# Performance work log

Hardware: AMD Instinct MI355X
Metric: run time of the kernel (lower is better)

Reference implementation:

```python
import jax, jax.numpy as jnp
import numpy as np

N_USERS = 100_000
N_ITEMS = 100_000
D = 64            # args.in_size == args.out_size (GraphConv has weight=None)
N_INTENTS = 128   # hardcoded in DCCF
HID = 128         # SemanticAttention hidden_size
N_UI_EDGES = 1_000_000
N_MP_EDGES = 500_000
N_MP = 2          # metapaths per node type
B = 4096
N_LAYERS = 2      # hardcoded in DCCF


def setup_inputs() -> dict:
    key = jax.random.key(0)
    ks = jax.random.split(key, 20)
    s = 0.1
    inp = {}
    inp['user_feat'] = jax.random.normal(ks[0], (N_USERS, D), jnp.float32) * s
    inp['item_feat'] = jax.random.normal(ks[1], (N_ITEMS, D), jnp.float32) * s
    inp['user_intent'] = jax.random.normal(ks[2], (D, N_INTENTS), jnp.float32) * s
    inp['item_intent'] = jax.random.normal(ks[3], (D, N_INTENTS), jnp.float32) * s
    inp['sa_u_W1'] = jax.random.normal(ks[4], (D, HID), jnp.float32) * s
    inp['sa_u_b1'] = jnp.zeros((HID,), jnp.float32)
    inp['sa_u_w2'] = jax.random.normal(ks[5], (HID,), jnp.float32) * s
    inp['sa_i_W1'] = jax.random.normal(ks[6], (D, HID), jnp.float32) * s
    inp['sa_i_b1'] = jnp.zeros((HID,), jnp.float32)
    inp['sa_i_w2'] = jax.random.normal(ks[7], (HID,), jnp.float32) * s
    inp['ui_src'] = jax.random.randint(ks[8], (N_UI_EDGES,), 0, N_USERS)
    inp['ui_dst'] = jax.random.randint(ks[9], (N_UI_EDGES,), 0, N_ITEMS)
    inp['mp_user'] = jax.random.randint(ks[10], (N_MP, 2, N_MP_EDGES), 0, N_USERS)
    inp['mp_item'] = jax.random.randint(ks[11], (N_MP, 2, N_MP_EDGES), 0, N_ITEMS)
    # indices drawn WITHOUT replacement so torch.unique(index) in ssl_loss is a no-op
    inp['user_idx'] = jax.random.choice(ks[12], N_USERS, (B,), replace=False)
    inp['item_idx'] = jax.random.choice(ks[13], N_ITEMS, (B,), replace=False)
    inp['neg_item_idx'] = jax.random.randint(ks[14], (B,), 0, N_ITEMS)
    return inp


def _forward(user_feat, item_feat, user_intent, item_intent,
             sa_u_W1, sa_u_b1, sa_u_w2, sa_i_W1, sa_i_b1, sa_i_w2,
             ui_src, ui_dst, mp_user, mp_item, user_idx, item_idx, neg_item_idx):
    n_nodes = N_USERS + N_ITEMS
    # symmetric bipartite adjacency in COO (tmp_adj + tmp_adj.T)
    rows = jnp.concatenate([ui_src, ui_dst + N_USERS])
    cols = jnp.concatenate([ui_dst + N_USERS, ui_src])
    deg = jnp.maximum(jax.ops.segment_sum(jnp.ones_like(rows, jnp.float32), rows,
                                          num_segments=n_nodes), 1.0)
    dinv = jax.lax.rsqrt(deg)
    gv = dinv[rows] * dinv[cols]  # G = D^{-1/2} A D^{-1/2}

    def spmm(x):  # gather-scale-scatter, the torch_sparse.spmm
        return jax.ops.segment_sum(gv[:, None] * x[cols], rows, num_segments=n_nodes)

    # ---- DCCF ----
    emb = jnp.concatenate([user_feat, item_feat], axis=0)
    total = emb
    for _ in range(N_LAYERS):
        gnn = spmm(emb)
        u, it = emb[:N_USERS], emb[N_USERS:]
        u_int = jax.nn.softmax(u @ user_intent, axis=1) @ user_intent.T
        i_int = jax.nn.softmax(it @ item_intent, axis=1) @ item_intent.T
        emb = gnn + jnp.concatenate([u_int, i_int], axis=0) + emb
        total = total + emb  # torch.stack(...).sum(dim=1)
    ua, ia = total[:N_USERS], total[N_USERS:]

    # ---- HANLayer: GraphConv(norm='both', weight=None) per metapath ----
    def graphconv(src, dst, h, n):
        ones = jnp.ones_like(src, jnp.float32)
        outdeg = jnp.maximum(jax.ops.segment_sum(ones, src, num_segments=n), 1.0)
        indeg = jnp.maximum(jax.ops.segment_sum(ones, dst, num_segments=n), 1.0)
        x = h * jax.lax.rsqrt(outdeg)[:, None]
        agg = jax.ops.segment_sum(x[src], dst, num_segments=n)
        return agg * jax.lax.rsqrt(indeg)[:, None]

    def sem_att(z, W1, b1, w2):  # z: [N, M, D]
        w = jnp.mean(jnp.tanh(z @ W1 + b1) @ w2, axis=0)  # [M]
        beta = jax.nn.softmax(w)
        return jnp.einsum('m,nmd->nd', beta, z)

    zu = jnp.stack([graphconv(mp_user[m, 0], mp_user[m, 1], user_feat, N_USERS)
                    for m in range(N_MP)], axis=1)
    h2_u = sem_att(zu, sa_u_W1, sa_u_b1, sa_u_w2)
    zi = jnp.stack([graphconv(mp_item[m, 0], mp_item[m, 1], item_feat, N_ITEMS)
                    for m in range(N_MP)], axis=1)
    h2_i = sem_att(zi, sa_i_W1, sa_i_b1, sa_i_w2)

    user_emb = 0.5 * ua + 0.5 * h2_u
    item_emb = 0.5 * ia + 0.5 * h2_i

    def ssl(d1, d2, idx):  # InfoNCE with temp 0.5 (idx already unique)
        e1 = d1[idx]
        e2 = d2[idx]
        e1 = e1 / jnp.linalg.norm(e1, axis=1, keepdims=True)
        e2 = e2 / jnp.linalg.norm(e2, axis=1, keepdims=True)
        pos = jnp.sum(e1 * e2, axis=1) / 0.5
        lse = jax.nn.logsumexp(e1 @ e2.T / 0.5, axis=1)
        return -jnp.sum(pos - lse) / idx.shape[0]

    ssl_loss = ssl(h2_u, ua, user_idx) + ssl(h2_i, ia, item_idx)
    return (user_emb[user_idx], item_emb[item_idx], item_emb[neg_item_idx], ssl_loss)


def reference(user_feat, item_feat, user_intent, item_intent,
              sa_u_W1, sa_u_b1, sa_u_w2, sa_i_W1, sa_i_b1, sa_i_w2,
              ui_src, ui_dst, mp_user, mp_item, user_idx, item_idx, neg_item_idx):
    return _forward(user_feat, item_feat, user_intent, item_intent,
                    sa_u_W1, sa_u_b1, sa_u_w2, sa_i_W1, sa_i_b1, sa_i_w2,
                    ui_src, ui_dst, mp_user, mp_item, user_idx, item_idx, neg_item_idx)
```

## Files before the change

kernel.cpp:

```cpp
#include <hip/hip_runtime.h>
#include <math.h>

#define NUSERS   100000
#define NITEMS   100000
#define NNODES   200000
#define DD       64
#define NI       128
#define E_UI     1000000
#define E_MP     500000
#define BB       4096
#define NSTRIP   6250

#define O_CNT       0LL
#define O_OUTCNT    600000LL
#define O_CURSOR    1000000LL
#define O_PARTIALS  1600000LL
#define O_UITB_U    1625600LL
#define O_UITB_I    1629696LL
#define O_UIB_U     1633792LL
#define O_UIB_I     1637888LL
#define O_W1B_U     1641984LL
#define O_W1B_I     1646080LL
#define O_SUMEXP    1700000LL
#define O_POS       1708192LL
#define ZEND        1716384LL
#define O_OFF       1716384LL
#define O_BSUM      2316448LL
#define O_DINV      2317472LL
#define O_OINV      2517472LL
#define O_IINV      2917472LL
#define O_ADJ       3317472LL
#define O_WSUM      7317472LL
#define O_EMBA      7317480LL
#define O_TOTAL     20117480LL
#define O_EMBB      32917480LL
#define O_E1U       45717480LL
#define O_E2U       45979624LL
#define O_E1I       46241768LL
#define O_E2I       46503912LL

typedef __attribute__((ext_vector_type(8))) short short8;
typedef __attribute__((ext_vector_type(4))) float f32x4;

__device__ __forceinline__ short f2bf(float x) {
  unsigned u = __float_as_uint(x);
  unsigned r = (u + 0x7FFFu + ((u >> 16) & 1u)) >> 16;
  return (short)r;
}

__global__ void k_hist_main(const int* __restrict__ src, const int* __restrict__ dst,
                            int* __restrict__ cnt) {
  int e = blockIdx.x * 256 + threadIdx.x;
  if (e < E_UI) {
    atomicAdd(&cnt[src[e]], 1);
    atomicAdd(&cnt[NUSERS + dst[e]], 1);
  }
}

__global__ void k_hist_mp(const int* __restrict__ mpu, const int* __restrict__ mpi,
                          int* __restrict__ cnt, int* __restrict__ outcnt) {
  int e = blockIdx.x * 256 + threadIdx.x;
  int g = blockIdx.y;
  if (e < E_MP) {
    const int* base = (g < 2) ? (mpu + (long long)g * 2 * E_MP)
                              : (mpi + (long long)(g - 2) * 2 * E_MP);
    int s = base[e];
    int d = base[E_MP + e];
    atomicAdd(&outcnt[g * NUSERS + s], 1);
    atomicAdd(&cnt[NNODES + g * NUSERS + d], 1);
  }
}

__global__ __launch_bounds__(1024) void k_scan1(const int* __restrict__ in, int* __restrict__ out,
                                                int* __restrict__ bsum, int n) {
  __shared__ int s[1024];
  int i = blockIdx.x * 1024 + threadIdx.x;
  int v = (i < n) ? in[i] : 0;
  s[threadIdx.x] = v;
  __syncthreads();
  for (int off = 1; off < 1024; off <<= 1) {
    int x = (threadIdx.x >= off) ? s[threadIdx.x - off] : 0;
    __syncthreads();
    s[threadIdx.x] += x;
    __syncthreads();
  }
  if (i < n) out[i] = s[threadIdx.x] - v;
  if (threadIdx.x == 1023) bsum[blockIdx.x] = s[1023];
}

__global__ __launch_bounds__(1024) void k_scan2(int* __restrict__ bsum, int nb) {
  __shared__ int s[1024];
  int v = (threadIdx.x < nb) ? bsum[threadIdx.x] : 0;
  s[threadIdx.x] = v;
  __syncthreads();
  for (int off = 1; off < 1024; off <<= 1) {
    int x = (threadIdx.x >= off) ? s[threadIdx.x - off] : 0;
    __syncthreads();
    s[threadIdx.x] += x;
    __syncthreads();
  }
  if (threadIdx.x < nb) bsum[threadIdx.x] = s[threadIdx.x] - v;
}

__global__ __launch_bounds__(1024) void k_scan3(int* __restrict__ out, const int* __restrict__ bsum, int n) {
  int i = blockIdx.x * 1024 + threadIdx.x;
  if (i < n) out[i] += bsum[blockIdx.x];
}

__global__ void k_inv(const int* __restrict__ cnt, const int* __restrict__ outcnt,
                      float* __restrict__ dinv, float* __restrict__ iinv, float* __restrict__ oinv) {
  int i = blockIdx.x * 256 + threadIdx.x;
  if (i < NNODES) {
    int c = cnt[i]; if (c < 1) c = 1;
    dinv[i] = 1.0f / sqrtf((float)c);
  } else if (i < 600000) {
    int c = cnt[i]; if (c < 1) c = 1;
    iinv[i - NNODES] = 1.0f / sqrtf((float)c);
  }
  if (i < 400000) {
    int c = outcnt[i]; if (c < 1) c = 1;
    oinv[i] = 1.0f / sqrtf((float)c);
  }
}

__global__ void k_scatter_main(const int* __restrict__ src, const int* __restrict__ dst,
                               const int* __restrict__ off, int* __restrict__ cursor,
                               int* __restrict__ adj) {
  int e = blockIdx.x * 256 + threadIdx.x;
  if (e < E_UI) {
    int u = src[e];
    int it = NUSERS + dst[e];
    int p = atomicAdd(&cursor[u], 1);
    adj[off[u] + p] = it;
    int q = atomicAdd(&cursor[it], 1);
    adj[off[it] + q] = u;
  }
}

__global__ void k_scatter_mp(const int* __restrict__ mpu, const int* __restrict__ mpi,
                             const int* __restrict__ off, int* __restrict__ cursor,
                             int* __restrict__ adj) {
  int e = blockIdx.x * 256 + threadIdx.x;
  int g = blockIdx.y;
  if (e < E_MP) {
    const int* base = (g < 2) ? (mpu + (long long)g * 2 * E_MP)
                              : (mpi + (long long)(g - 2) * 2 * E_MP);
    int s = base[e];
    int d = base[E_MP + e];
    int node = NNODES + g * NUSERS + d;
    int p = atomicAdd(&cursor[node], 1);
    adj[off[node] + p] = s;
  }
}

__global__ void k_init(const float4* __restrict__ uf, const float4* __restrict__ itf,
                       float4* __restrict__ emb) {
  int i = blockIdx.x * 256 + threadIdx.x;
  if (i < 3200000) {
    emb[i] = (i < 1600000) ? uf[i] : itf[i - 1600000];
  }
}

__global__ void k_tw(const float* __restrict__ UIu, const float* __restrict__ UIi,
                     const float* __restrict__ W1u, const float* __restrict__ W1i,
                     short* __restrict__ UITBu, short* __restrict__ UITBi,
                     short* __restrict__ UIBu,  short* __restrict__ UIBi,
                     short* __restrict__ W1Bu,  short* __restrict__ W1Bi) {
  int t = blockIdx.x * 256 + threadIdx.x;
  if (t < 8192) {
    int d = t >> 7, j = t & 127;
    UITBu[j * 64 + d] = f2bf(UIu[t]);
    UITBi[j * 64 + d] = f2bf(UIi[t]);
    UIBu[t] = f2bf(UIu[t]);
    UIBi[t] = f2bf(UIi[t]);
    W1Bu[j * 64 + d] = f2bf(W1u[t]);
    W1Bi[j * 64 + d] = f2bf(W1i[t]);
  }
}

__device__ __forceinline__ float acc8(const float* __restrict__ tbl, int miv, float mwv,
                                      int rem, int lane, float acc) {
  unsigned wb = __float_as_uint(mwv);
  for (int k = 0; k < rem; k += 8) {
    int n0 = __builtin_amdgcn_readlane(miv, k + 0);
    int n1 = __builtin_amdgcn_readlane(miv, k + 1);
    int n2 = __builtin_amdgcn_readlane(miv, k + 2);
    int n3 = __builtin_amdgcn_readlane(miv, k + 3);
    int n4 = __builtin_amdgcn_readlane(miv, k + 4);
    int n5 = __builtin_amdgcn_readlane(miv, k + 5);
    int n6 = __builtin_amdgcn_readlane(miv, k + 6);
    int n7 = __builtin_amdgcn_readlane(miv, k + 7);
    float w0 = __uint_as_float(__builtin_amdgcn_readlane(wb, k + 0));
    float w1 = __uint_as_float(__builtin_amdgcn_readlane(wb, k + 1));
    float w2 = __uint_as_float(__builtin_amdgcn_readlane(wb, k + 2));
    float w3 = __uint_as_float(__builtin_amdgcn_readlane(wb, k + 3));
    float w4 = __uint_as_float(__builtin_amdgcn_readlane(wb, k + 4));
    float w5 = __uint_as_float(__builtin_amdgcn_readlane(wb, k + 5));
    float w6 = __uint_as_float(__builtin_amdgcn_readlane(wb, k + 6));
    float w7 = __uint_as_float(__builtin_amdgcn_readlane(wb, k + 7));
    float v0 = tbl[((long long)n0 << 6) + lane], v1 = tbl[((long long)n1 << 6) + lane];
    float v2 = tbl[((long long)n2 << 6) + lane], v3 = tbl[((long long)n3 << 6) + lane];
    float v4 = tbl[((long long)n4 << 6) + lane], v5 = tbl[((long long)n5 << 6) + lane];
    float v6 = tbl[((long long)n6 << 6) + lane], v7 = tbl[((long long)n7 << 6) + lane];
    acc += w0 * v0; acc += w1 * v1; acc += w2 * v2; acc += w3 * v3;
    acc += w4 * v4; acc += w5 * v5; acc += w6 * v6; acc += w7 * v7;
  }
  return acc;
}

template <int R>
__device__ __forceinline__ float acc8f(const float* __restrict__ tbl, int miv, float mwv,
                                       int lane) {
  unsigned wb = __float_as_uint(mwv);
  float acc = 0.0f;
#pragma unroll
  for (int k = 0; k < R; k += 8) {
    int n0 = __builtin_amdgcn_readlane(miv, k + 0);
    int n1 = __builtin_amdgcn_readlane(miv, k + 1);
    int n2 = __builtin_amdgcn_readlane(miv, k + 2);
    int n3 = __builtin_amdgcn_readlane(miv, k + 3);
    int n4 = __builtin_amdgcn_readlane(miv, k + 4);
    int n5 = __builtin_amdgcn_readlane(miv, k + 5);
    int n6 = __builtin_amdgcn_readlane(miv, k + 6);
    int n7 = __builtin_amdgcn_readlane(miv, k + 7);
    float w0 = __uint_as_float(__builtin_amdgcn_readlane(wb, k + 0));
    float w1 = __uint_as_float(__builtin_amdgcn_readlane(wb, k + 1));
    float w2 = __uint_as_float(__builtin_amdgcn_readlane(wb, k + 2));
    float w3 = __uint_as_float(__builtin_amdgcn_readlane(wb, k + 3));
    float w4 = __uint_as_float(__builtin_amdgcn_readlane(wb, k + 4));
    float w5 = __uint_as_float(__builtin_amdgcn_readlane(wb, k + 5));
    float w6 = __uint_as_float(__builtin_amdgcn_readlane(wb, k + 6));
    float w7 = __uint_as_float(__builtin_amdgcn_readlane(wb, k + 7));
    float v0 = tbl[((long long)n0 << 6) + lane], v1 = tbl[((long long)n1 << 6) + lane];
    float v2 = tbl[((long long)n2 << 6) + lane], v3 = tbl[((long long)n3 << 6) + lane];
    float v4 = tbl[((long long)n4 << 6) + lane], v5 = tbl[((long long)n5 << 6) + lane];
    float v6 = tbl[((long long)n6 << 6) + lane], v7 = tbl[((long long)n7 << 6) + lane];
    acc += w0 * v0; acc += w1 * v1; acc += w2 * v2; acc += w3 * v3;
    acc += w4 * v4; acc += w5 * v5; acc += w6 * v6; acc += w7 * v7;
  }
  return acc;
}

__device__ __forceinline__ float gather_tail(const float* __restrict__ tbl,
                                             const int* __restrict__ adj,
                                             int start, int c,
                                             const float* __restrict__ warr, int wofs,
                                             int lane, float acc) {
  for (int kb = 64; kb < c; kb += 64) {
    int rem = c - kb; if (rem > 64) rem = 64;
    int ti = 0; float tw = 0.0f;
    if (lane < rem) { ti = adj[start + kb + lane]; tw = warr[wofs + ti]; }
    acc = acc8(tbl, ti, tw, rem, lane, acc);
  }
  return acc;
}

__device__ __forceinline__ float gather_node(const float* __restrict__ tbl,
                                             const int* __restrict__ adj,
                                             int ofs, int c, int miv, float mwv,
                                             const float* __restrict__ warr, int wofs,
                                             int lane) {
  if (c <= 8)  return acc8f<8>(tbl, miv, mwv, lane);
  if (c <= 16) return acc8f<16>(tbl, miv, mwv, lane);
  if (c <= 24) return acc8f<24>(tbl, miv, mwv, lane);
  int rem = c < 64 ? c : 64;
  float acc = acc8(tbl, miv, mwv, rem, lane, 0.0f);
  if (c > 64) acc = gather_tail(tbl, adj, ofs, c, warr, wofs, lane, acc);
  return acc;
}

__device__ __forceinline__ void acc4x(const float* __restrict__ tbl, int miv, float mwv,
                                      int rem, int grp, int dq, f32x4& acc) {
  for (int k = 0; k < rem; k += 16) {
    int s0 = k + grp, s1 = k + 4 + grp, s2 = k + 8 + grp, s3 = k + 12 + grp;
    int n0 = __shfl(miv, s0), n1 = __shfl(miv, s1);
    int n2 = __shfl(miv, s2), n3 = __shfl(miv, s3);
    float w0 = __shfl(mwv, s0), w1 = __shfl(mwv, s1);
    float w2 = __shfl(mwv, s2), w3 = __shfl(mwv, s3);
    float4 v0 = *(const float4*)(tbl + ((long long)n0 << 6) + dq);
    float4 v1 = *(const float4*)(tbl + ((long long)n1 << 6) + dq);
    float4 v2 = *(const float4*)(tbl + ((long long)n2 << 6) + dq);
    float4 v3 = *(const float4*)(tbl + ((long long)n3 << 6) + dq);
    acc.x += w0 * v0.x; acc.y += w0 * v0.y; acc.z += w0 * v0.z; acc.w += w0 * v0.w;
    acc.x += w1 * v1.x; acc.y += w1 * v1.y; acc.z += w1 * v1.z; acc.w += w1 * v1.w;
    acc.x += w2 * v2.x; acc.y += w2 * v2.y; acc.z += w2 * v2.z; acc.w += w2 * v2.w;
    acc.x += w3 * v3.x; acc.y += w3 * v3.y; acc.z += w3 * v3.z; acc.w += w3 * v3.w;
  }
}

__device__ __forceinline__ void gather_tail4(const float* __restrict__ tbl,
                                             const int* __restrict__ adj,
                                             int start, int c,
                                             const float* __restrict__ warr, int wofs,
                                             int lane, int grp, int dq, f32x4& acc) {
  for (int kb = 64; kb < c; kb += 64) {
    int rem = c - kb; if (rem > 64) rem = 64;
    int ti = 0; float tw = 0.0f;
    if (lane < rem) { ti = adj[start + kb + lane]; tw = warr[wofs + ti]; }
    acc4x(tbl, ti, tw, rem, grp, dq, acc);
  }
}

__device__ __forceinline__ float bcastf(float x) {
  return __uint_as_float(__builtin_amdgcn_readfirstlane(__float_as_uint(x)));
}

__global__ __launch_bounds__(128, 4) void k_layer(
    const float* __restrict__ ecur, float* __restrict__ enext, float* __restrict__ total,
    const int* __restrict__ adj, const int* __restrict__ off, const int* __restrict__ cnt,
    const float* __restrict__ dinv,
    const short* __restrict__ UITBu, const short* __restrict__ UITBi,
    const short* __restrict__ UIBu,  const short* __restrict__ UIBi, int layer) {
  __shared__ float sZ[2][16 * 68];
  __shared__ short sP[2][16 * 136];
  int w = threadIdx.x >> 6, lane = threadIdx.x & 63;
  int nb = blockIdx.x * 32 + w * 16;
  const short* UITB = (nb < NUSERS) ? UITBu : UITBi;
  const short* UIB  = (nb < NUSERS) ? UIBu  : UIBi;
  float* rowZ = sZ[w];
  short* rowP = sP[w];
  int quad = lane >> 4, mrow = lane & 15;

  const float* vrow = ecur + (((long long)(nb + mrow)) << 6) + quad * 8;
  float4 va0 = *(const float4*)(vrow);
  float4 va1 = *(const float4*)(vrow + 4);
  float4 vc0 = *(const float4*)(vrow + 32);
  float4 vc1 = *(const float4*)(vrow + 36);
  short8 a0 = { f2bf(va0.x), f2bf(va0.y), f2bf(va0.z), f2bf(va0.w),
                f2bf(va1.x), f2bf(va1.y), f2bf(va1.z), f2bf(va1.w) };
  short8 a1 = { f2bf(vc0.x), f2bf(vc0.y), f2bf(vc0.z), f2bf(vc0.w),
                f2bf(vc1.x), f2bf(vc1.y), f2bf(vc1.z), f2bf(vc1.w) };

  {
    int ofs[16], cns[16];
    float dn[16];
    int mi[16]; float mw[16];
#pragma unroll
    for (int m = 0; m < 16; m++) {
      ofs[m] = __builtin_amdgcn_readfirstlane(off[nb + m]);
      cns[m] = __builtin_amdgcn_readfirstlane(cnt[nb + m]);
      dn[m]  = bcastf(dinv[nb + m]);
    }
#pragma unroll
    for (int m = 0; m < 16; m++)
      mi[m] = (lane < cns[m]) ? adj[ofs[m] + lane] : 0;
#pragma unroll
    for (int m = 0; m < 16; m++)
      mw[m] = (lane < cns[m]) ? dinv[mi[m]] : 0.0f;
#pragma unroll
    for (int m = 0; m < 16; m++) {
      float acc = gather_node(ecur, adj, ofs[m], cns[m], mi[m], mw[m], dinv, 0, lane);
      rowZ[m * 68 + lane] = dn[m] * acc;
    }
  }

  float den0 = 0.f, den1 = 0.f, den2 = 0.f, den3 = 0.f;
  short* pw = rowP + (quad * 4) * 136 + mrow;
#pragma unroll
  for (int jt = 0; jt < 8; jt++) {
    const short* wr = UITB + ((jt * 16 + mrow) << 6) + quad * 8;
    short8 b0 = *(const short8*)(wr);
    short8 bh = *(const short8*)(wr + 32);
    f32x4 acc = {0.f, 0.f, 0.f, 0.f};
    acc = __builtin_amdgcn_mfma_f32_16x16x32_bf16(a0, b0, acc, 0, 0, 0);
    acc = __builtin_amdgcn_mfma_f32_16x16x32_bf16(a1, bh, acc, 0, 0, 0);
    float e0 = __expf(acc[0]), e1 = __expf(acc[1]);
    float e2 = __expf(acc[2]), e3 = __expf(acc[3]);
    den0 += e0; den1 += e1; den2 += e2; den3 += e3;
    short* pj = pw + jt * 16;
    pj[0] = f2bf(e0); pj[136] = f2bf(e1); pj[272] = f2bf(e2); pj[408] = f2bf(e3);
  }
  for (int mask = 1; mask <= 8; mask <<= 1) {
    den0 += __shfl_xor(den0, mask); den1 += __shfl_xor(den1, mask);
    den2 += __shfl_xor(den2, mask); den3 += __shfl_xor(den3, mask);
  }
  float rd0 = 1.f / den0, rd1 = 1.f / den1, rd2 = 1.f / den2, rd3 = 1.f / den3;

#pragma unroll
  for (int dt = 0; dt < 4; dt++) {
    f32x4 acc = {0.f, 0.f, 0.f, 0.f};
#pragma unroll
    for (int c = 0; c < 4; c++) {
      const short* pr = rowP + mrow * 136 + c * 32 + quad * 8;
      short8 af = *(const short8*)(pr);
      const short* br = UIB + ((dt * 16 + mrow) << 7) + c * 32 + quad * 8;
      short8 bf = *(const short8*)(br);
      acc = __builtin_amdgcn_mfma_f32_16x16x32_bf16(af, bf, acc, 0, 0, 0);
    }
    int d = dt * 16 + mrow;
#define COMB(r, rd)                                                            \
    { int node = nb + quad * 4 + r;                                            \
      long long base = (((long long)node) << 6) + d;                           \
      float o = acc[r] * rd;                                                   \
      float gn = rowZ[(quad * 4 + r) * 68 + d];                                \
      float vv = ecur[base];                                                   \
      float ne = gn + o + vv;                                                  \
      enext[base] = ne;                                                        \
      total[base] = (layer == 0) ? (vv + ne) : (total[base] + ne); }
    COMB(0, rd0) COMB(1, rd1) COMB(2, rd2) COMB(3, rd3)
#undef COMB
  }
}

__global__ __launch_bounds__(256, 6) void k_mp_gather(
    const float* __restrict__ uf, const float* __restrict__ itf,
    const int* __restrict__ adj, const int* __restrict__ off, const int* __restrict__ cnt,
    const float* __restrict__ oinv, const float* __restrict__ iinv,
    float* __restrict__ zu, float* __restrict__ zi) {
  int g = blockIdx.y;
  const float* feat = (g < 2) ? uf : itf;
  float* zb = (g < 2) ? zu + ((long long)g * NUSERS << 6)
                      : zi + ((long long)(g - 2) * NUSERS << 6);
  int w = threadIdx.x >> 6, lane = threadIdx.x & 63;
  int n0 = (blockIdx.x * 4 + w) * 4;
  int gofs = g * NUSERS;
  int grp = lane >> 4, dq = (lane & 15) << 2;
  int ofs[4], cns[4];
  float iv[4];
  int mi[4]; float mw[4];
#pragma unroll
  for (int m = 0; m < 4; m++) {
    int node = NNODES + gofs + n0 + m;
    ofs[m] = __builtin_amdgcn_readfirstlane(off[node]);
    cns[m] = __builtin_amdgcn_readfirstlane(cnt[node]);
    iv[m]  = bcastf(iinv[gofs + n0 + m]);
  }
#pragma unroll
  for (int m = 0; m < 4; m++)
    mi[m] = (lane < cns[m]) ? adj[ofs[m] + lane] : 0;
#pragma unroll
  for (int m = 0; m < 4; m++)
    mw[m] = (lane < cns[m]) ? oinv[gofs + mi[m]] : 0.0f;
#pragma unroll
  for (int m = 0; m < 4; m++) {
    int c = cns[m];
    f32x4 acc = {0.f, 0.f, 0.f, 0.f};
    if (c <= 16) {
      acc4x(feat, mi[m], mw[m], 16, grp, dq, acc);
    } else {
      int rem = c < 64 ? c : 64;
      acc4x(feat, mi[m], mw[m], rem, grp, dq, acc);
      if (c > 64) gather_tail4(feat, adj, ofs[m], c, oinv, gofs, lane, grp, dq, acc);
    }
    acc.x += __shfl_xor(acc.x, 16); acc.y += __shfl_xor(acc.y, 16);
    acc.z += __shfl_xor(acc.z, 16); acc.w += __shfl_xor(acc.w, 16);
    acc.x += __shfl_xor(acc.x, 32); acc.y += __shfl_xor(acc.y, 32);
    acc.z += __shfl_xor(acc.z, 32); acc.w += __shfl_xor(acc.w, 32);
    if (lane < 16) {
      float s = iv[m];
      float4 o = { acc.x * s, acc.y * s, acc.z * s, acc.w * s };
      *(float4*)&zb[((long long)(n0 + m) << 6) + dq] = o;
    }
  }
}

__global__ __launch_bounds__(256, 4) void k_mp_mlp(
    const float* __restrict__ zu, const float* __restrict__ zi,
    const short* __restrict__ W1Bu, const float* __restrict__ b1u, const float* __restrict__ w2u,
    const short* __restrict__ W1Bi, const float* __restrict__ b1i, const float* __restrict__ w2i,
    float* __restrict__ partials) {
  int g = blockIdx.y;
  const short* W1B = (g < 2) ? W1Bu : W1Bi;
  const float* b1  = (g < 2) ? b1u : b1i;
  const float* w2  = (g < 2) ? w2u : w2i;
  const float* zb  = (g < 2) ? zu + ((long long)g * NUSERS << 6)
                             : zi + ((long long)(g - 2) * NUSERS << 6);
  int w = threadIdx.x >> 6, lane = threadIdx.x & 63;
  int strip = blockIdx.x * 4 + w;
  if (strip >= NSTRIP) return;
  int quad = lane >> 4, mrow = lane & 15;
  const float* zrow = zb + (((long long)(strip * 16 + mrow)) << 6) + quad * 8;
  float4 za0 = *(const float4*)(zrow);
  float4 za1 = *(const float4*)(zrow + 4);
  float4 zc0 = *(const float4*)(zrow + 32);
  float4 zc1 = *(const float4*)(zrow + 36);
  short8 a0 = { f2bf(za0.x), f2bf(za0.y), f2bf(za0.z), f2bf(za0.w),
                f2bf(za1.x), f2bf(za1.y), f2bf(za1.z), f2bf(za1.w) };
  short8 a1 = { f2bf(zc0.x), f2bf(zc0.y), f2bf(zc0.z), f2bf(zc0.w),
                f2bf(zc1.x), f2bf(zc1.y), f2bf(zc1.z), f2bf(zc1.w) };
  float psum = 0.0f;
#pragma unroll
  for (int jt = 0; jt < 8; jt++) {
    const short* wr = W1B + ((jt * 16 + mrow) << 6) + quad * 8;
    short8 b0 = *(const short8*)(wr);
    short8 bh = *(const short8*)(wr + 32);
    f32x4 acc = {0.f, 0.f, 0.f, 0.f};
    acc = __builtin_amdgcn_mfma_f32_16x16x32_bf16(a0, b0, acc, 0, 0, 0);
    acc = __builtin_amdgcn_mfma_f32_16x16x32_bf16(a1, bh, acc, 0, 0, 0);
    int j = jt * 16 + mrow;
    float bj = b1[j], wj = w2[j];
#pragma unroll
    for (int r = 0; r < 4; r++) {
      float s = acc[r] + bj;
      psum += wj * (1.0f - 2.0f / (__expf(2.0f * s) + 1.0f));
    }
  }
  for (int m = 32; m; m >>= 1) psum += __shfl_xor(psum, m);
  if (lane == 0) partials[g * NSTRIP + strip] = psum;
}

__global__ void k_beta(const float* __restrict__ partials, float* __restrict__ wsum) {
  int g = blockIdx.x;
  float s = 0.0f;
  for (int i = threadIdx.x; i < NSTRIP; i += 256) s += partials[g * NSTRIP + i];
  for (int m = 32; m; m >>= 1) s += __shfl_xor(s, m);
  __shared__ float r[4];
  if ((threadIdx.x & 63) == 0) r[threadIdx.x >> 6] = s;
  __syncthreads();
  if (threadIdx.x == 0) wsum[g] = r[0] + r[1] + r[2] + r[3];
}

__global__ __launch_bounds__(256) void k_h2out(
    const float* __restrict__ zu, const float* __restrict__ zi,
    const int* __restrict__ user_idx, const int* __restrict__ item_idx, const int* __restrict__ neg_idx,
    const float* __restrict__ total,
    const float* __restrict__ wsum, float* __restrict__ out,
    short* __restrict__ e1u, short* __restrict__ e2u,
    short* __restrict__ e1i, short* __restrict__ e2i, float* __restrict__ pos) {
  int lane = threadIdx.x & 63;
  int row = (blockIdx.x << 2) + (threadIdx.x >> 6);
  int seg = row >> 12;
  int r = row & 4095;
  int idx;
  const float* zb;
  int gbase;
  if (seg == 0)      { idx = user_idx[r]; zb = zu; gbase = 0; }
  else if (seg == 1) { idx = item_idx[r]; zb = zi; gbase = 2; }
  else               { idx = neg_idx[r];  zb = zi; gbase = 2; }
  int tnode = gbase ? (NUSERS + idx) : idx;
  float t = total[((long long)tnode << 6) + lane];
  float w0 = wsum[gbase] * (1.0f / 100000.0f);
  float w1 = wsum[gbase + 1] * (1.0f / 100000.0f);
  float mb = fmaxf(w0, w1);
  float b0 = expf(w0 - mb), b1 = expf(w1 - mb);
  float bs = b0 + b1;
  b0 /= bs; b1 /= bs;
  float z0 = zb[((long long)idx << 6) + lane];
  float z1 = zb[(((long long)NUSERS + idx) << 6) + lane];
  float h2 = b0 * z0 + b1 * z1;
  out[((long long)row << 6) + lane] = 0.5f * t + 0.5f * h2;
  if (seg < 2) {
    float n1 = h2 * h2, n2 = t * t;
    for (int m = 32; m; m >>= 1) { n1 += __shfl_xor(n1, m); n2 += __shfl_xor(n2, m); }
    n1 = sqrtf(n1); n2 = sqrtf(n2);
    float a = h2 / n1, b = t / n2;
    float d = a * b;
    for (int m = 32; m; m >>= 1) d += __shfl_xor(d, m);
    short* e1 = seg ? e1i : e1u;
    short* e2 = seg ? e2i : e2u;
    e1[((long long)r << 6) + lane] = f2bf(a);
    e2[((long long)r << 6) + lane] = f2bf(b);
    if (lane == 0) pos[seg * BB + r] = 2.0f * d;
  }
}

__global__ __launch_bounds__(256) void k_gemm(const short* __restrict__ e1u, const short* __restrict__ e2u,
                                              const short* __restrict__ e1i, const short* __restrict__ e2i,
                                              float* __restrict__ sumexp) {
  int side = blockIdx.z;
  const short* A = side ? e1i : e1u;
  const short* B = side ? e2i : e2u;
  int w = threadIdx.x >> 6, lane = threadIdx.x & 63;
  int quad = lane >> 4, mrow = lane & 15;
  int rbase = blockIdx.y * 64;
  int cbase = blockIdx.x * 256 + w * 64;

  short8 a0[4], a1[4], b0[4], b1[4];
#pragma unroll
  for (int ri = 0; ri < 4; ri++) {
    const short* ar = A + ((long long)(rbase + ri * 16 + mrow) << 6) + quad * 8;
    a0[ri] = *(const short8*)ar;
    a1[ri] = *(const short8*)(ar + 32);
  }
#pragma unroll
  for (int ci = 0; ci < 4; ci++) {
    const short* br = B + ((long long)(cbase + ci * 16 + mrow) << 6) + quad * 8;
    b0[ci] = *(const short8*)br;
    b1[ci] = *(const short8*)(br + 32);
  }
  float rs0[4] = {0.f, 0.f, 0.f, 0.f};
  float rs1[4] = {0.f, 0.f, 0.f, 0.f};
  float rs2[4] = {0.f, 0.f, 0.f, 0.f};
  float rs3[4] = {0.f, 0.f, 0.f, 0.f};
#pragma unroll
  for (int ri = 0; ri < 4; ri++) {
#pragma unroll
    for (int ci = 0; ci < 4; ci++) {
      f32x4 acc = {0.f, 0.f, 0.f, 0.f};
      acc = __builtin_amdgcn_mfma_f32_16x16x32_bf16(a0[ri], b0[ci], acc, 0, 0, 0);
      acc = __builtin_amdgcn_mfma_f32_16x16x32_bf16(a1[ri], b1[ci], acc, 0, 0, 0);
      float e0 = __expf(2.0f * acc[0]);
      float e1 = __expf(2.0f * acc[1]);
      float e2 = __expf(2.0f * acc[2]);
      float e3 = __expf(2.0f * acc[3]);
      if (ri == 0) { rs0[0] += e0; rs0[1] += e1; rs0[2] += e2; rs0[3] += e3; }
      if (ri == 1) { rs1[0] += e0; rs1[1] += e1; rs1[2] += e2; rs1[3] += e3; }
      if (ri == 2) { rs2[0] += e0; rs2[1] += e1; rs2[2] += e2; rs2[3] += e3; }
      if (ri == 3) { rs3[0] += e0; rs3[1] += e1; rs3[2] += e2; rs3[3] += e3; }
    }
  }
#pragma unroll
  for (int mask = 1; mask <= 8; mask <<= 1) {
#pragma unroll
    for (int r = 0; r < 4; r++) {
      rs0[r] += __shfl_xor(rs0[r], mask);
      rs1[r] += __shfl_xor(rs1[r], mask);
      rs2[r] += __shfl_xor(rs2[r], mask);
      rs3[r] += __shfl_xor(rs3[r], mask);
    }
  }
  if (mrow == 0) {
    float* sb = sumexp + side * BB + rbase + quad * 4;
#pragma unroll
    for (int r = 0; r < 4; r++) {
      __hip_atomic_fetch_add(&sb[r], rs0[r], __ATOMIC_RELAXED, __HIP_MEMORY_SCOPE_AGENT);
      __hip_atomic_fetch_add(&sb[16 + r], rs1[r], __ATOMIC_RELAXED, __HIP_MEMORY_SCOPE_AGENT);
      __hip_atomic_fetch_add(&sb[32 + r], rs2[r], __ATOMIC_RELAXED, __HIP_MEMORY_SCOPE_AGENT);
      __hip_atomic_fetch_add(&sb[48 + r], rs3[r], __ATOMIC_RELAXED, __HIP_MEMORY_SCOPE_AGENT);
    }
  }
}

__global__ void k_loss(const float* __restrict__ sumexp, const float* __restrict__ pos,
                       float* __restrict__ out) {
  float s = 0.0f;
  for (int i = threadIdx.x; i < 2 * BB; i += 256) s += logf(sumexp[i]) - pos[i];
  for (int m = 32; m; m >>= 1) s += __shfl_xor(s, m);
  __shared__ float r[4];
  if ((threadIdx.x & 63) == 0) r[threadIdx.x >> 6] = s;
  __syncthreads();
  if (threadIdx.x == 0) out[3 * BB * DD] = (r[0] + r[1] + r[2] + r[3]) * (1.0f / (float)BB);
}

extern "C" void kernel_launch(void* const* d_in, const int* in_sizes, int n_in,
                              void* d_out, int out_size, void* d_ws, size_t ws_size,
                              hipStream_t stream) {
  const float* uf  = (const float*)d_in[0];
  const float* itf = (const float*)d_in[1];
  const float* UIu = (const float*)d_in[2];
  const float* UIi = (const float*)d_in[3];
  const float* W1u = (const float*)d_in[4];
  const float* b1u = (const float*)d_in[5];
  const float* w2u = (const float*)d_in[6];
  const float* W1i = (const float*)d_in[7];
  const float* b1i = (const float*)d_in[8];
  const float* w2i = (const float*)d_in[9];
  const int* ui_src   = (const int*)d_in[10];
  const int* ui_dst   = (const int*)d_in[11];
  const int* mpu      = (const int*)d_in[12];
  const int* mpi      = (const int*)d_in[13];
  const int* user_idx = (const int*)d_in[14];
  const int* item_idx = (const int*)d_in[15];
  const int* neg_idx  = (const int*)d_in[16];
  float* out = (float*)d_out;

  float* wf = (float*)d_ws;
  int*   wi = (int*)d_ws;

  int*   cnt      = wi + O_CNT;
  int*   outcnt   = wi + O_OUTCNT;
  int*   cursor   = wi + O_CURSOR;
  float* partials = wf + O_PARTIALS;
  short* UITBu    = (short*)(wf + O_UITB_U);
  short* UITBi    = (short*)(wf + O_UITB_I);
  short* UIBu     = (short*)(wf + O_UIB_U);
  short* UIBi     = (short*)(wf + O_UIB_I);
  short* W1Bu     = (short*)(wf + O_W1B_U);
  short* W1Bi     = (short*)(wf + O_W1B_I);
  float* sumexp   = wf + O_SUMEXP;
  float* pos      = wf + O_POS;
  int*   off      = wi + O_OFF;
  int*   bsum     = wi + O_BSUM;
  float* dinv     = wf + O_DINV;
  float* oinv     = wf + O_OINV;
  float* iinv     = wf + O_IINV;
  int*   adj      = wi + O_ADJ;
  float* wsum     = wf + O_WSUM;
  float* emba     = wf + O_EMBA;
  float* total    = wf + O_TOTAL;
  float* embb     = wf + O_EMBB;
  short* e1u      = (short*)(wf + O_E1U);
  short* e2u      = (short*)(wf + O_E2U);
  short* e1i      = (short*)(wf + O_E1I);
  short* e2i      = (short*)(wf + O_E2I);

  hipMemsetAsync(d_ws, 0, (size_t)ZEND * 4, stream);

  k_hist_main<<<(E_UI + 255) / 256, 256, 0, stream>>>(ui_src, ui_dst, cnt);
  k_hist_mp<<<dim3((E_MP + 255) / 256, 4), 256, 0, stream>>>(mpu, mpi, cnt, outcnt);

  const int NSCAN = 600000;
  const int NB = (NSCAN + 1023) / 1024;
  k_scan1<<<NB, 1024, 0, stream>>>(cnt, off, bsum, NSCAN);
  k_scan2<<<1, 1024, 0, stream>>>(bsum, NB);
  k_scan3<<<NB, 1024, 0, stream>>>(off, bsum, NSCAN);

  k_inv<<<(600000 + 255) / 256, 256, 0, stream>>>(cnt, outcnt, dinv, iinv, oinv);

  k_scatter_main<<<(E_UI + 255) / 256, 256, 0, stream>>>(ui_src, ui_dst, off, cursor, adj);
  k_scatter_mp<<<dim3((E_MP + 255) / 256, 4), 256, 0, stream>>>(mpu, mpi, off, cursor, adj);

  k_init<<<(3200000 + 255) / 256, 256, 0, stream>>>((const float4*)uf, (const float4*)itf,
                                                    (float4*)emba);
  k_tw<<<32, 256, 0, stream>>>(UIu, UIi, W1u, W1i, UITBu, UITBi, UIBu, UIBi, W1Bu, W1Bi);

  k_layer<<<6250, 128, 0, stream>>>(emba, embb, total, adj, off, cnt, dinv,
                                    UITBu, UITBi, UIBu, UIBi, 0);
  k_layer<<<6250, 128, 0, stream>>>(embb, emba, total, adj, off, cnt, dinv,
                                    UITBu, UITBi, UIBu, UIBi, 1);

  k_mp_gather<<<dim3(6250, 4), 256, 0, stream>>>(uf, itf, adj, off, cnt, oinv, iinv,
                                                 emba, embb);
  k_mp_mlp<<<dim3((NSTRIP + 3) / 4, 4), 256, 0, stream>>>(emba, embb, W1Bu, b1u, w2u,
                                                          W1Bi, b1i, w2i, partials);
  k_beta<<<4, 256, 0, stream>>>(partials, wsum);

  k_h2out<<<3072, 256, 0, stream>>>(emba, embb, user_idx, item_idx, neg_idx, total,
                                    wsum, out, e1u, e2u, e1i, e2i, pos);

  k_gemm<<<dim3(16, 64, 2), 256, 0, stream>>>(e1u, e2u, e1i, e2i, sumexp);
  k_loss<<<1, 256, 0, stream>>>(sumexp, pos, out);
}
```

Before: 1.134 ms.

## Fuse metapath gather with semantic-attention MLP and specialize gather by strip max degree

Merges the metapath neighbour gather and the semantic-attention MLP into one kernel. Each wave gathers 16 nodes into shared memory and feeds the MFMA directly from LDS, so the MLP no longer re-reads z from global memory and one launch is saved. Both the layer kernel and the fused kernel now take the strip's maximum degree and pick a fixed-size unrolled gather for the whole strip, which removes per-node branching. In exchange the gather switches from 4-wide float4 lanes to the scalar per-lane acc8f path, and each block now carries more registers and LDS.

```diff
diff --git a/kernel.cpp b/kernel.cpp
--- a/kernel.cpp
+++ b/kernel.cpp
@@ -269,38 +269,6 @@
   return acc;
 }
 
-__device__ __forceinline__ void acc4x(const float* __restrict__ tbl, int miv, float mwv,
-                                      int rem, int grp, int dq, f32x4& acc) {
-  for (int k = 0; k < rem; k += 16) {
-    int s0 = k + grp, s1 = k + 4 + grp, s2 = k + 8 + grp, s3 = k + 12 + grp;
-    int n0 = __shfl(miv, s0), n1 = __shfl(miv, s1);
-    int n2 = __shfl(miv, s2), n3 = __shfl(miv, s3);
-    float w0 = __shfl(mwv, s0), w1 = __shfl(mwv, s1);
-    float w2 = __shfl(mwv, s2), w3 = __shfl(mwv, s3);
-    float4 v0 = *(const float4*)(tbl + ((long long)n0 << 6) + dq);
-    float4 v1 = *(const float4*)(tbl + ((long long)n1 << 6) + dq);
-    float4 v2 = *(const float4*)(tbl + ((long long)n2 << 6) + dq);
-    float4 v3 = *(const float4*)(tbl + ((long long)n3 << 6) + dq);
-    acc.x += w0 * v0.x; acc.y += w0 * v0.y; acc.z += w0 * v0.z; acc.w += w0 * v0.w;
-    acc.x += w1 * v1.x; acc.y += w1 * v1.y; acc.z += w1 * v1.z; acc.w += w1 * v1.w;
-    acc.x += w2 * v2.x; acc.y += w2 * v2.y; acc.z += w2 * v2.z; acc.w += w2 * v2.w;
-    acc.x += w3 * v3.x; acc.y += w3 * v3.y; acc.z += w3 * v3.z; acc.w += w3 * v3.w;
-  }
-}
-
-__device__ __forceinline__ void gather_tail4(const float* __restrict__ tbl,
-                                             const int* __restrict__ adj,
-                                             int start, int c,
-                                             const float* __restrict__ warr, int wofs,
-                                             int lane, int grp, int dq, f32x4& acc) {
-  for (int kb = 64; kb < c; kb += 64) {
-    int rem = c - kb; if (rem > 64) rem = 64;
-    int ti = 0; float tw = 0.0f;
-    if (lane < rem) { ti = adj[start + kb + lane]; tw = warr[wofs + ti]; }
-    acc4x(tbl, ti, tw, rem, grp, dq, acc);
-  }
-}
-
 __device__ __forceinline__ float bcastf(float x) {
   return __uint_as_float(__builtin_amdgcn_readfirstlane(__float_as_uint(x)));
 }
@@ -335,11 +303,13 @@
     int ofs[16], cns[16];
     float dn[16];
     int mi[16]; float mw[16];
+    int cmax = 0;
 #pragma unroll
     for (int m = 0; m < 16; m++) {
       ofs[m] = __builtin_amdgcn_readfirstlane(off[nb + m]);
       cns[m] = __builtin_amdgcn_readfirstlane(cnt[nb + m]);
       dn[m]  = bcastf(dinv[nb + m]);
+      cmax = cns[m] > cmax ? cns[m] : cmax;
     }
 #pragma unroll
     for (int m = 0; m < 16; m++)
@@ -347,10 +317,25 @@
 #pragma unroll
     for (int m = 0; m < 16; m++)
       mw[m] = (lane < cns[m]) ? dinv[mi[m]] : 0.0f;
-#pragma unroll
-    for (int m = 0; m < 16; m++) {
-      float acc = gather_node(ecur, adj, ofs[m], cns[m], mi[m], mw[m], dinv, 0, lane);
-      rowZ[m * 68 + lane] = dn[m] * acc;
+
+    if (cmax <= 16) {
+#pragma unroll
+      for (int m = 0; m < 16; m++) {
+        float acc = acc8f<16>(ecur, mi[m], mw[m], lane);
+        rowZ[m * 68 + lane] = dn[m] * acc;
+      }
+    } else if (cmax <= 24) {
+#pragma unroll
+      for (int m = 0; m < 16; m++) {
+        float acc = acc8f<24>(ecur, mi[m], mw[m], lane);
+        rowZ[m * 68 + lane] = dn[m] * acc;
+      }
+    } else {
+#pragma unroll
+      for (int m = 0; m < 16; m++) {
+        float acc = gather_node(ecur, adj, ofs[m], cns[m], mi[m], mw[m], dinv, 0, lane);
+        rowZ[m * 68 + lane] = dn[m] * acc;
+      }
     }
   }
 
@@ -402,82 +387,79 @@
   }
 }
 
-__global__ __launch_bounds__(256, 6) void k_mp_gather(
+__global__ __launch_bounds__(128, 4) void k_mp_fused(
     const float* __restrict__ uf, const float* __restrict__ itf,
     const int* __restrict__ adj, const int* __restrict__ off, const int* __restrict__ cnt,
     const float* __restrict__ oinv, const float* __restrict__ iinv,
-    float* __restrict__ zu, float* __restrict__ zi) {
+    float* __restrict__ zu, float* __restrict__ zi,
+    const short* __restrict__ W1Bu, const float* __restrict__ b1u, const float* __restrict__ w2u,
+    const short* __restrict__ W1Bi, const float* __restrict__ b1i, const float* __restrict__ w2i,
+    float* __restrict__ partials) {
+  __shared__ float sZ[2][16 * 68];
   int g = blockIdx.y;
   const float* feat = (g < 2) ? uf : itf;
   float* zb = (g < 2) ? zu + ((long long)g * NUSERS << 6)
                       : zi + ((long long)(g - 2) * NUSERS << 6);
-  int w = threadIdx.x >> 6, lane = threadIdx.x & 63;
-  int n0 = (blockIdx.x * 4 + w) * 4;
-  int gofs = g * NUSERS;
-  int grp = lane >> 4, dq = (lane & 15) << 2;
-  int ofs[4], cns[4];
-  float iv[4];
-  int mi[4]; float mw[4];
-#pragma unroll
-  for (int m = 0; m < 4; m++) {
-    int node = NNODES + gofs + n0 + m;
-    ofs[m] = __builtin_amdgcn_readfirstlane(off[node]);
-    cns[m] = __builtin_amdgcn_readfirstlane(cnt[node]);
-    iv[m]  = bcastf(iinv[gofs + n0 + m]);
-  }
-#pragma unroll
-  for (int m = 0; m < 4; m++)
-    mi[m] = (lane < cns[m]) ? adj[ofs[m] + lane] : 0;
-#pragma unroll
-  for (int m = 0; m < 4; m++)
-    mw[m] = (lane < cns[m]) ? oinv[gofs + mi[m]] : 0.0f;
-#pragma unroll
-  for (int m = 0; m < 4; m++) {
-    int c = cns[m];
-    f32x4 acc = {0.f, 0.f, 0.f, 0.f};
-    if (c <= 16) {
-      acc4x(feat, mi[m], mw[m], 16, grp, dq, acc);
-    } else {
-      int rem = c < 64 ? c : 64;
-      acc4x(feat, mi[m], mw[m], rem, grp, dq, acc);
-      if (c > 64) gather_tail4(feat, adj, ofs[m], c, oinv, gofs, lane, grp, dq, acc);
-    }
-    acc.x += __shfl_xor(acc.x, 16); acc.y += __shfl_xor(acc.y, 16);
-    acc.z += __shfl_xor(acc.z, 16); acc.w += __shfl_xor(acc.w, 16);
-    acc.x += __shfl_xor(acc.x, 32); acc.y += __shfl_xor(acc.y, 32);
-    acc.z += __shfl_xor(acc.z, 32); acc.w += __shfl_xor(acc.w, 32);
-    if (lane < 16) {
-      float s = iv[m];
-      float4 o = { acc.x * s, acc.y * s, acc.z * s, acc.w * s };
-      *(float4*)&zb[((long long)(n0 + m) << 6) + dq] = o;
-    }
-  }
-}
-
-__global__ __launch_bounds__(256, 4) void k_mp_mlp(
-    const float* __restrict__ zu, const float* __restrict__ zi,
-    const short* __restrict__ W1Bu, const float* __restrict__ b1u, const float* __restrict__ w2u,
-    const short* __restrict__ W1Bi, const float* __restrict__ b1i, const float* __restrict__ w2i,
-    float* __restrict__ partials) {
-  int g = blockIdx.y;
   const short* W1B = (g < 2) ? W1Bu : W1Bi;
   const float* b1  = (g < 2) ? b1u : b1i;
   const float* w2  = (g < 2) ? w2u : w2i;
-  const float* zb  = (g < 2) ? zu + ((long long)g * NUSERS << 6)
-                             : zi + ((long long)(g - 2) * NUSERS << 6);
   int w = threadIdx.x >> 6, lane = threadIdx.x & 63;
-  int strip = blockIdx.x * 4 + w;
-  if (strip >= NSTRIP) return;
+  int strip = blockIdx.x * 2 + w;
+  int nb = strip * 16;
+  int gofs = g * NUSERS;
+  float* rowZ = sZ[w];
+
+  {
+    int ofs[16], cns[16];
+    float dn[16];
+    int mi[16]; float mw[16];
+    int cmax = 0;
+#pragma unroll
+    for (int m = 0; m < 16; m++) {
+      int node = NNODES + gofs + nb + m;
+      ofs[m] = __builtin_amdgcn_readfirstlane(off[node]);
+      cns[m] = __builtin_amdgcn_readfirstlane(cnt[node]);
+      dn[m]  = bcastf(iinv[gofs + nb + m]);
+      cmax = cns[m] > cmax ? cns[m] : cmax;
+    }
+#pragma unroll
+    for (int m = 0; m < 16; m++)
+      mi[m] = (lane < cns[m]) ? adj[ofs[m] + lane] : 0;
+#pragma unroll
+    for (int m = 0; m < 16; m++)
+      mw[m] = (lane < cns[m]) ? oinv[gofs + mi[m]] : 0.0f;
+
+    if (cmax <= 8) {
+#pragma unroll
+      for (int m = 0; m < 16; m++) {
+        float zv = dn[m] * acc8f<8>(feat, mi[m], mw[m], lane);
+        rowZ[m * 68 + lane] = zv;
+        zb[((long long)(nb + m) << 6) + lane] = zv;
+      }
+    } else if (cmax <= 16) {
+#pragma unroll
+      for (int m = 0; m < 16; m++) {
+        float zv = dn[m] * acc8f<16>(feat, mi[m], mw[m], lane);
+        rowZ[m * 68 + lane] = zv;
+        zb[((long long)(nb + m) << 6) + lane] = zv;
+      }
+    } else {
+#pragma unroll
+      for (int m = 0; m < 16; m++) {
+        float zv = dn[m] * gather_node(feat, adj, ofs[m], cns[m], mi[m], mw[m],
+                                       oinv, gofs, lane);
+        rowZ[m * 68 + lane] = zv;
+        zb[((long long)(nb + m) << 6) + lane] = zv;
+      }
+    }
+  }
+
   int quad = lane >> 4, mrow = lane & 15;
-  const float* zrow = zb + (((long long)(strip * 16 + mrow)) << 6) + quad * 8;
-  float4 za0 = *(const float4*)(zrow);
-  float4 za1 = *(const float4*)(zrow + 4);
-  float4 zc0 = *(const float4*)(zrow + 32);
-  float4 zc1 = *(const float4*)(zrow + 36);
-  short8 a0 = { f2bf(za0.x), f2bf(za0.y), f2bf(za0.z), f2bf(za0.w),
-                f2bf(za1.x), f2bf(za1.y), f2bf(za1.z), f2bf(za1.w) };
-  short8 a1 = { f2bf(zc0.x), f2bf(zc0.y), f2bf(zc0.z), f2bf(zc0.w),
-                f2bf(zc1.x), f2bf(zc1.y), f2bf(zc1.z), f2bf(zc1.w) };
+  const float* zrow = rowZ + mrow * 68 + quad * 8;
+  short8 a0 = { f2bf(zrow[0]), f2bf(zrow[1]), f2bf(zrow[2]), f2bf(zrow[3]),
+                f2bf(zrow[4]), f2bf(zrow[5]), f2bf(zrow[6]), f2bf(zrow[7]) };
+  short8 a1 = { f2bf(zrow[32]), f2bf(zrow[33]), f2bf(zrow[34]), f2bf(zrow[35]),
+                f2bf(zrow[36]), f2bf(zrow[37]), f2bf(zrow[38]), f2bf(zrow[39]) };
   float psum = 0.0f;
 #pragma unroll
   for (int jt = 0; jt < 8; jt++) {
@@ -709,10 +691,9 @@
   k_layer<<<6250, 128, 0, stream>>>(embb, emba, total, adj, off, cnt, dinv,
                                     UITBu, UITBi, UIBu, UIBi, 1);
 
-  k_mp_gather<<<dim3(6250, 4), 256, 0, stream>>>(uf, itf, adj, off, cnt, oinv, iinv,
-                                                 emba, embb);
-  k_mp_mlp<<<dim3((NSTRIP + 3) / 4, 4), 256, 0, stream>>>(emba, embb, W1Bu, b1u, w2u,
-                                                          W1Bi, b1i, w2i, partials);
+  k_mp_fused<<<dim3(3125, 4), 128, 0, stream>>>(uf, itf, adj, off, cnt, oinv, iinv,
+                                                emba, embb,
+                                                W1Bu, b1u, w2u, W1Bi, b1i, w2i, partials);
   k_beta<<<4, 256, 0, stream>>>(partials, wsum);
 
   k_h2out<<<3072, 256, 0, stream>>>(emba, embb, user_idx, item_idx, neg_idx, total,
```

Measured after the change: 1.101 ms. -2.9%, faster.
